# Optimization experiments

Hardware: AMD Instinct MI355X
Metric: run time of the kernel (lower is better)

## Reference

```python
import jax, jax.numpy as jnp
import numpy as np

D, H, NL, DFF, VS, VT = 512, 8, 6, 2048, 32000, 32000
B, SS, ST = 4, 512, 512
PAD = 1
EPS = 1e-5


def _pos_encoding(S, d):
    pos = jnp.arange(S, dtype=jnp.float32)[:, None]
    div = jnp.exp(jnp.arange(0, d, 2, dtype=jnp.float32) * (-jnp.log(jnp.float32(10000.0)) / d))
    pe = jnp.zeros((S, d), dtype=jnp.float32)
    pe = pe.at[:, 0::2].set(jnp.sin(pos * div))
    pe = pe.at[:, 1::2].set(jnp.cos(pos * div))
    return pe


def _ln(x, g, b):
    m = jnp.mean(x, axis=-1, keepdims=True)
    v = jnp.mean(jnp.square(x - m), axis=-1, keepdims=True)
    return (x - m) * jax.lax.rsqrt(v + EPS) * g + b


def _mha(q, k, v, Wq, Wk, Wv, Wo, mask):
    # q,k,v: [B,S,D]; W*: [D,D] (torch Linear: y = x @ W.T); mask True -> masked
    Bq, Sq, _ = q.shape
    Sk = k.shape[1]
    dk = D // H
    Q = (q @ Wq.T).reshape(Bq, Sq, H, dk).transpose(0, 2, 1, 3)
    K = (k @ Wk.T).reshape(Bq, Sk, H, dk).transpose(0, 2, 1, 3)
    V = (v @ Wv.T).reshape(Bq, Sk, H, dk).transpose(0, 2, 1, 3)
    scores = jnp.einsum('bhqd,bhkd->bhqk', Q, K) / jnp.sqrt(jnp.float32(dk))
    scores = jnp.where(mask, -jnp.inf, scores)
    w = jax.nn.softmax(scores, axis=-1)
    w = jnp.nan_to_num(w)  # matches torch.nan_to_num after softmax of all -inf rows
    out = jnp.einsum('bhqk,bhkd->bhqd', w, V)
    out = out.transpose(0, 2, 1, 3).reshape(Bq, Sq, D)
    return out @ Wo.T


def _ffn(x, w1, b1, w2, b2):
    return jax.nn.relu(x @ w1.T + b1) @ w2.T + b2


def setup_inputs() -> dict:
    key = jax.random.key(0)
    ks = jax.random.split(key, 48)
    i = iter(range(48))
    n = lambda shape, s=0.02: jax.random.normal(ks[next(i)], shape, dtype=jnp.float32) * s
    inp = {
        'src': jax.random.randint(ks[next(i)], (B, SS), 0, VS),
        'tgt': jax.random.randint(ks[next(i)], (B, ST), 0, VT),
        'src_embed': n((VS, D)),
        'tgt_embed': n((VT, D)),
        'enc_Wq': n((NL, D, D)), 'enc_Wk': n((NL, D, D)), 'enc_Wv': n((NL, D, D)), 'enc_Wo': n((NL, D, D)),
        'enc_w1': n((NL, DFF, D)), 'enc_b1': jnp.zeros((NL, DFF)),
        'enc_w2': n((NL, D, DFF)), 'enc_b2': jnp.zeros((NL, D)),
        'enc_ln1g': jnp.ones((NL, D)), 'enc_ln1b': jnp.zeros((NL, D)),
        'enc_ln2g': jnp.ones((NL, D)), 'enc_ln2b': jnp.zeros((NL, D)),
        'enc_lnfg': jnp.ones((D,)), 'enc_lnfb': jnp.zeros((D,)),
        'dec_sWq': n((NL, D, D)), 'dec_sWk': n((NL, D, D)), 'dec_sWv': n((NL, D, D)), 'dec_sWo': n((NL, D, D)),
        'dec_cWq': n((NL, D, D)), 'dec_cWk': n((NL, D, D)), 'dec_cWv': n((NL, D, D)), 'dec_cWo': n((NL, D, D)),
        'dec_w1': n((NL, DFF, D)), 'dec_b1': jnp.zeros((NL, DFF)),
        'dec_w2': n((NL, D, DFF)), 'dec_b2': jnp.zeros((NL, D)),
        'dec_ln1g': jnp.ones((NL, D)), 'dec_ln1b': jnp.zeros((NL, D)),
        'dec_ln2g': jnp.ones((NL, D)), 'dec_ln2b': jnp.zeros((NL, D)),
        'dec_ln3g': jnp.ones((NL, D)), 'dec_ln3b': jnp.zeros((NL, D)),
        'dec_lnfg': jnp.ones((D,)), 'dec_lnfb': jnp.zeros((D,)),
        'out_W': n((VT, D)), 'out_b': jnp.zeros((VT,)),
    }
    return inp


def reference(src, tgt, src_embed, tgt_embed,
              enc_Wq, enc_Wk, enc_Wv, enc_Wo, enc_w1, enc_b1, enc_w2, enc_b2,
              enc_ln1g, enc_ln1b, enc_ln2g, enc_ln2b, enc_lnfg, enc_lnfb,
              dec_sWq, dec_sWk, dec_sWv, dec_sWo, dec_cWq, dec_cWk, dec_cWv, dec_cWo,
              dec_w1, dec_b1, dec_w2, dec_b2,
              dec_ln1g, dec_ln1b, dec_ln2g, dec_ln2b, dec_ln3g, dec_ln3b,
              dec_lnfg, dec_lnfb, out_W, out_b):
    scale = jnp.sqrt(jnp.float32(D))
    src_mask = (src == PAD)[:, None, None, :]                      # [B,1,1,SS]
    causal = jnp.triu(jnp.ones((ST, ST), dtype=bool), k=1)[None, None]
    tgt_mask = (tgt == PAD)[:, None, None, :] | causal             # [B,1,ST,ST]

    # Encoder
    x = src_embed[src] * scale + _pos_encoding(SS, D)[None]
    for l in range(NL):
        nrm = _ln(x, enc_ln1g[l], enc_ln1b[l])
        x = x + _mha(nrm, nrm, nrm, enc_Wq[l], enc_Wk[l], enc_Wv[l], enc_Wo[l], src_mask)
        x = x + _ffn(_ln(x, enc_ln2g[l], enc_ln2b[l]), enc_w1[l], enc_b1[l], enc_w2[l], enc_b2[l])
    memory = _ln(x, enc_lnfg, enc_lnfb)

    # Decoder
    y = tgt_embed[tgt] * scale + _pos_encoding(ST, D)[None]
    for l in range(NL):
        nrm = _ln(y, dec_ln1g[l], dec_ln1b[l])
        y = y + _mha(nrm, nrm, nrm, dec_sWq[l], dec_sWk[l], dec_sWv[l], dec_sWo[l], tgt_mask)
        nrm = _ln(y, dec_ln2g[l], dec_ln2b[l])
        y = y + _mha(nrm, memory, memory, dec_cWq[l], dec_cWk[l], dec_cWv[l], dec_cWo[l], src_mask)
        y = y + _ffn(_ln(y, dec_ln3g[l], dec_ln3b[l]), dec_w1[l], dec_b1[l], dec_w2[l], dec_b2[l])
    y = _ln(y, dec_lnfg, dec_lnfb)

    logits = y @ out_W.T + out_b                                   # [B,ST,VT]
    return logits
```

## Files before the change

### kernel.cpp

```cpp
#include <hip/hip_runtime.h>
#include <hip/hip_bf16.h>
#include <math.h>

#define Dm    512
#define Hh    8
#define NLay  6
#define DFFm  2048
#define Bb    4
#define NTOK  2048
#define PADID 1
#define LNEPS 1e-5f
#define S2W   262144

typedef __attribute__((ext_vector_type(8))) short short8;
typedef __attribute__((ext_vector_type(4))) float f32x4;
typedef unsigned short u16;

__device__ __forceinline__ u16 f2bf(float f) {
    union { float f; unsigned int i; } x; x.f = f;
    unsigned int r = x.i + 0x7fffu + ((x.i >> 16) & 1u);
    return (u16)(r >> 16);
}

typedef const __attribute__((address_space(1))) void* as1cv;
typedef __attribute__((address_space(3))) void* as3v;
__device__ __forceinline__ void gl_lds16(const u16* g, u16* l) {
    __builtin_amdgcn_global_load_lds((as1cv)g, (as3v)l, 16, 0, 0);
}

__device__ __forceinline__ void swz_tile(int& mt, int& nt) {
    const int nwg  = gridDim.x * gridDim.y;
    const int orig = blockIdx.y * gridDim.x + blockIdx.x;
    const int q8 = nwg >> 3, r8 = nwg & 7;
    const int xcd = orig & 7, idx = orig >> 3;
    const int wgid = (xcd < r8 ? xcd * (q8 + 1) : r8 * (q8 + 1) + (xcd - r8) * q8) + idx;
    const int MT = gridDim.y;
    mt = wgid % MT;
    nt = wgid / MT;
}

struct CvtJobs {
    const float* s[17];
    u16*         d[17];
    long         n4[17];
};
__global__ __launch_bounds__(256) void cvt_many(CvtJobs j) {
    const int job = blockIdx.y;
    const long n4 = j.n4[job];
    const float* in = j.s[job];
    u16* out = j.d[job];
    long i = (long)blockIdx.x * 256 + threadIdx.x;
    const long stride = (long)gridDim.x * 256;
    for (; i < n4; i += stride) {
        float4 v = ((const float4*)in)[i];
        ushort4 o;
        o.x = f2bf(v.x); o.y = f2bf(v.y); o.z = f2bf(v.z); o.w = f2bf(v.w);
        ((ushort4*)out)[i] = o;
    }
}

__global__ __launch_bounds__(256) void gemm_bt(
    const u16* __restrict__ A, int lda,
    const u16* __restrict__ B0, const u16* __restrict__ B1,
    const u16* __restrict__ B2, int ldb,
    float* Cf, u16* Cb, int csm,
    const float* __restrict__ bias,
    const float* res, int ldres,
    int K, int vth, int koff, u16* vtp)
{
    __shared__ u16 As[2][2048];
    __shared__ u16 Bs[2][2048];
    int mt, nt; swz_tile(mt, nt);
    const int m0 = mt << 6, n0 = nt << 6;
    const int t = threadIdx.x, lane = t & 63, wave = t >> 6;
    const int wr = (wave >> 1) << 5, wc = (wave & 1) << 5;
    const int fr = lane & 15, fq = lane >> 4;
    const int srow = t >> 2;
    const int sch  = (t & 3) ^ (srow & 3);
    const u16* Bsel = (n0 < 512) ? B0 : (n0 < 1024 ? B1 : B2);
    const u16* Ag = A + (long)(m0 + srow) * lda + (sch << 3);
    const u16* Bg = Bsel + (long)((n0 & 511) + srow) * ldb + (sch << 3);

    f32x4 acc[2][2];
    #pragma unroll
    for (int i = 0; i < 2; i++)
        #pragma unroll
        for (int j = 0; j < 2; j++) acc[i][j] = (f32x4){0.f, 0.f, 0.f, 0.f};

    const int nk = K >> 5;
    gl_lds16(Ag, &As[0][t << 3]);
    gl_lds16(Bg, &Bs[0][t << 3]);
    for (int ki = 0; ki < nk; ki++) {
        const int cur = ki & 1;
        __syncthreads();
        if (ki + 1 < nk) {
            gl_lds16(Ag + ((ki + 1) << 5), &As[cur ^ 1][t << 3]);
            gl_lds16(Bg + ((ki + 1) << 5), &Bs[cur ^ 1][t << 3]);
        }
        const int r0 = wr + fr, r1 = wr + 16 + fr;
        const int c0 = wc + fr, c1 = wc + 16 + fr;
        short8 af0 = *(const short8*)&As[cur][(r0 << 5) + ((fq ^ (r0 & 3)) << 3)];
        short8 af1 = *(const short8*)&As[cur][(r1 << 5) + ((fq ^ (r1 & 3)) << 3)];
        short8 bf0 = *(const short8*)&Bs[cur][(c0 << 5) + ((fq ^ (c0 & 3)) << 3)];
        short8 bf1 = *(const short8*)&Bs[cur][(c1 << 5) + ((fq ^ (c1 & 3)) << 3)];
        acc[0][0] = __builtin_amdgcn_mfma_f32_16x16x32_bf16(af0, bf0, acc[0][0], 0, 0, 0);
        acc[0][1] = __builtin_amdgcn_mfma_f32_16x16x32_bf16(af0, bf1, acc[0][1], 0, 0, 0);
        acc[1][0] = __builtin_amdgcn_mfma_f32_16x16x32_bf16(af1, bf0, acc[1][0], 0, 0, 0);
        acc[1][1] = __builtin_amdgcn_mfma_f32_16x16x32_bf16(af1, bf1, acc[1][1], 0, 0, 0);
        __syncthreads();
    }

    #pragma unroll
    for (int i = 0; i < 2; i++) {
        #pragma unroll
        for (int j = 0; j < 2; j++) {
            const int nl  = n0 + wc + (j << 4) + fr;
            const int mlb = m0 + wr + (i << 4) + (fq << 2);
            const float bsv = bias ? bias[nl] : 0.f;
            #pragma unroll
            for (int r = 0; r < 4; r++) {
                const int ml = mlb + r;
                float v = acc[i][j][r] + bsv;
                if (nl >= vth) {
                    vtp[(long)(ml >> 9) * S2W + (long)(nl - vth) * 512 + (ml & 511)] = f2bf(v);
                } else {
                    long ci = (long)ml * csm + nl + koff;
                    if (res) v += res[(long)ml * ldres + nl];
                    if (Cf) Cf[ci] = v;
                    if (Cb) Cb[ci] = f2bf(v);
                }
            }
        }
    }
}

__global__ __launch_bounds__(256) void gemm_big(
    const u16* __restrict__ A, int lda,
    const u16* __restrict__ B, int ldb,
    float* Cf, u16* Cb, int ldc,
    const float* __restrict__ bias, int relu, int K)
{
    __shared__ u16 As[2][4096];
    __shared__ u16 Bs[2][4096];
    int mt, nt; swz_tile(mt, nt);
    const int m0 = mt << 7, n0 = nt << 7;
    const int t = threadIdx.x, lane = t & 63, wave = t >> 6;
    const int wr = (wave >> 1) << 6, wc = (wave & 1) << 6;
    const int fr = lane & 15, fq = lane >> 4;
    const int srow = t >> 2;
    const int sch  = (t & 3) ^ (srow & 3);
    const u16* Ag0 = A + (long)(m0 + srow) * lda + (sch << 3);
    const u16* Ag1 = A + (long)(m0 + 64 + srow) * lda + (sch << 3);
    const u16* Bg0 = B + (long)(n0 + srow) * ldb + (sch << 3);
    const u16* Bg1 = B + (long)(n0 + 64 + srow) * ldb + (sch << 3);

    f32x4 acc[4][4];
    #pragma unroll
    for (int i = 0; i < 4; i++)
        #pragma unroll
        for (int j = 0; j < 4; j++) acc[i][j] = (f32x4){0.f, 0.f, 0.f, 0.f};

    const int nk = K >> 5;
    gl_lds16(Ag0, &As[0][t << 3]);
    gl_lds16(Ag1, &As[0][2048 + (t << 3)]);
    gl_lds16(Bg0, &Bs[0][t << 3]);
    gl_lds16(Bg1, &Bs[0][2048 + (t << 3)]);
    for (int ki = 0; ki < nk; ki++) {
        const int cur = ki & 1;
        __syncthreads();
        if (ki + 1 < nk) {
            const int ko = (ki + 1) << 5;
            gl_lds16(Ag0 + ko, &As[cur ^ 1][t << 3]);
            gl_lds16(Ag1 + ko, &As[cur ^ 1][2048 + (t << 3)]);
            gl_lds16(Bg0 + ko, &Bs[cur ^ 1][t << 3]);
            gl_lds16(Bg1 + ko, &Bs[cur ^ 1][2048 + (t << 3)]);
        }
        short8 af[4], bf[4];
        #pragma unroll
        for (int i = 0; i < 4; i++) {
            const int r = wr + (i << 4) + fr;
            af[i] = *(const short8*)&As[cur][(r << 5) + ((fq ^ (r & 3)) << 3)];
        }
        #pragma unroll
        for (int j = 0; j < 4; j++) {
            const int c = wc + (j << 4) + fr;
            bf[j] = *(const short8*)&Bs[cur][(c << 5) + ((fq ^ (c & 3)) << 3)];
        }
        #pragma unroll
        for (int i = 0; i < 4; i++)
            #pragma unroll
            for (int j = 0; j < 4; j++)
                acc[i][j] = __builtin_amdgcn_mfma_f32_16x16x32_bf16(af[i], bf[j], acc[i][j], 0, 0, 0);
        __syncthreads();
    }

    #pragma unroll
    for (int i = 0; i < 4; i++) {
        #pragma unroll
        for (int j = 0; j < 4; j++) {
            const int nl  = n0 + wc + (j << 4) + fr;
            const int mlb = m0 + wr + (i << 4) + (fq << 2);
            const float bsv = bias ? bias[nl] : 0.f;
            #pragma unroll
            for (int r = 0; r < 4; r++) {
                float v = acc[i][j][r] + bsv;
                if (relu) v = fmaxf(v, 0.f);
                long ci = (long)(mlb + r) * ldc + nl;
                if (Cf) Cf[ci] = v;
                if (Cb) Cb[ci] = f2bf(v);
            }
        }
    }
}

__global__ __launch_bounds__(256) void attn_fused(
    const u16* __restrict__ qkb, const u16* __restrict__ vt,
    const int* __restrict__ ids, u16* __restrict__ attc, int causal)
{
    __shared__ u16 Ks[2][4096];
    __shared__ u16 Vs[2][4096];
    __shared__ short Ps[4][16][72];
    const int t = threadIdx.x, lane = t & 63, w = t >> 6;
    const int fr = lane & 15, fq = lane >> 4;
    const int q0 = blockIdx.x << 6, h = blockIdx.y, b = blockIdx.z;

    const u16* qp = qkb + (long)(b * 512 + q0 + (w << 4) + fr) * 1024 + h * 64 + (fq << 3);
    short8 aq0 = *(const short8*)qp;
    short8 aq1 = *(const short8*)(qp + 32);

    const int sr0 = t >> 3,        sc0 = (t & 7) ^ (sr0 & 7);
    const int sr1 = (t + 256) >> 3, sc1 = ((t + 256) & 7) ^ (sr1 & 7);
    const u16* kg0 = qkb + (long)(b * 512 + sr0) * 1024 + 512 + h * 64 + (sc0 << 3);
    const u16* kg1 = qkb + (long)(b * 512 + sr1) * 1024 + 512 + h * 64 + (sc1 << 3);
    const u16* vg0 = vt + (long)b * S2W + (long)(h * 64 + sr0) * 512 + (sc0 << 3);
    const u16* vg1 = vt + (long)b * S2W + (long)(h * 64 + sr1) * 512 + (sc1 << 3);

    unsigned pmask = 0;
    #pragma unroll
    for (int kt = 0; kt < 8; kt++)
        #pragma unroll
        for (int j = 0; j < 4; j++)
            if (ids[b * 512 + (kt << 6) + (j << 4) + fr] == PADID)
                pmask |= 1u << ((kt << 2) + j);

    float m[4], l[4]; f32x4 oc[4];
    #pragma unroll
    for (int r = 0; r < 4; r++) { m[r] = -INFINITY; l[r] = 0.f; oc[r] = (f32x4){0.f,0.f,0.f,0.f}; }

    const int lastkt = causal ? (q0 >> 6) : 7;
    auto stage = [&](int kt, int buf) {
        const long so = (long)(kt << 6);
        gl_lds16(kg0 + so * 1024, &Ks[buf][t << 3]);
        gl_lds16(kg1 + so * 1024, &Ks[buf][(t + 256) << 3]);
        gl_lds16(vg0 + so, &Vs[buf][t << 3]);
        gl_lds16(vg1 + so, &Vs[buf][(t + 256) << 3]);
    };
    stage(0, 0);

    for (int kt = 0; kt <= lastkt; kt++) {
        const int cur = kt & 1;
        __syncthreads();
        if (kt < lastkt) stage(kt + 1, cur ^ 1);

        f32x4 sc[4];
        #pragma unroll
        for (int j = 0; j < 4; j++) sc[j] = (f32x4){0.f,0.f,0.f,0.f};
        #pragma unroll
        for (int j = 0; j < 4; j++) {
            const int rr = (j << 4) + fr;
            short8 bk0 = *(const short8*)&Ks[cur][rr * 64 + ((fq ^ (rr & 7)) << 3)];
            short8 bk1 = *(const short8*)&Ks[cur][rr * 64 + (((fq | 4) ^ (rr & 7)) << 3)];
            sc[j] = __builtin_amdgcn_mfma_f32_16x16x32_bf16(aq0, bk0, sc[j], 0, 0, 0);
            sc[j] = __builtin_amdgcn_mfma_f32_16x16x32_bf16(aq1, bk1, sc[j], 0, 0, 0);
        }
        const int s0 = kt << 6;
        #pragma unroll
        for (int r = 0; r < 4; r++) {
            const int qa = q0 + (w << 4) + (fq << 2) + r;
            float mx = -INFINITY;
            #pragma unroll
            for (int j = 0; j < 4; j++) {
                bool msk = ((pmask >> ((kt << 2) + j)) & 1) ||
                           (causal && (s0 + (j << 4) + fr) > qa);
                float sv = msk ? -INFINITY : sc[j][r] * 0.125f;
                sc[j][r] = sv;
                mx = fmaxf(mx, sv);
            }
            mx = fmaxf(mx, __shfl_xor(mx, 1)); mx = fmaxf(mx, __shfl_xor(mx, 2));
            mx = fmaxf(mx, __shfl_xor(mx, 4)); mx = fmaxf(mx, __shfl_xor(mx, 8));
            float mnew  = fmaxf(m[r], mx);
            float scale = (mnew == -INFINITY) ? 1.f : __expf(m[r] - mnew);
            float ps = 0.f;
            #pragma unroll
            for (int j = 0; j < 4; j++) {
                float p = (sc[j][r] == -INFINITY) ? 0.f : __expf(sc[j][r] - mnew);
                sc[j][r] = p; ps += p;
            }
            ps += __shfl_xor(ps, 1); ps += __shfl_xor(ps, 2);
            ps += __shfl_xor(ps, 4); ps += __shfl_xor(ps, 8);
            l[r] = l[r] * scale + ps;
            m[r] = mnew;
            #pragma unroll
            for (int j2 = 0; j2 < 4; j2++) oc[j2][r] *= scale;
        }
        #pragma unroll
        for (int r = 0; r < 4; r++)
            #pragma unroll
            for (int j = 0; j < 4; j++)
                Ps[w][(fq << 2) + r][(j << 4) + fr] = (short)f2bf(sc[j][r]);
        #pragma unroll
        for (int kc = 0; kc < 2; kc++) {
            short8 pa = *(const short8*)&Ps[w][fr][(kc << 5) + (fq << 3)];
            #pragma unroll
            for (int j2 = 0; j2 < 4; j2++) {
                const int rd = (j2 << 4) + fr;
                const int cch = (((kc << 2) | fq) ^ (rd & 7));
                short8 bv = *(const short8*)&Vs[cur][rd * 64 + (cch << 3)];
                oc[j2] = __builtin_amdgcn_mfma_f32_16x16x32_bf16(pa, bv, oc[j2], 0, 0, 0);
            }
        }
        __syncthreads();
    }

    float inv[4];
    #pragma unroll
    for (int r = 0; r < 4; r++) inv[r] = (l[r] > 0.f) ? 1.f / l[r] : 0.f;
    #pragma unroll
    for (int j2 = 0; j2 < 4; j2++)
        #pragma unroll
        for (int r = 0; r < 4; r++)
            attc[(long)(b * 512 + q0 + (w << 4) + (fq << 2) + r) * 512 + h * 64 + (j2 << 4) + fr]
                = f2bf(oc[j2][r] * inv[r]);
}

__global__ __launch_bounds__(256) void ln_rows(
    const float* __restrict__ x, const float* __restrict__ g,
    const float* __restrict__ b, u16* __restrict__ out)
{
    int row  = blockIdx.x * 4 + (threadIdx.x >> 6);
    int lane = threadIdx.x & 63;
    const float* xr = x + (long)row * Dm;
    float v[8]; float s = 0.f;
    #pragma unroll
    for (int i = 0; i < 8; i++) { v[i] = xr[lane + (i << 6)]; s += v[i]; }
    #pragma unroll
    for (int o = 32; o > 0; o >>= 1) s += __shfl_xor(s, o);
    float mean = s * (1.f / 512.f);
    float q = 0.f;
    #pragma unroll
    for (int i = 0; i < 8; i++) { float d = v[i] - mean; q += d * d; }
    #pragma unroll
    for (int o = 32; o > 0; o >>= 1) q += __shfl_xor(q, o);
    float rinv = rsqrtf(q * (1.f / 512.f) + LNEPS);
    u16* orow = out + (long)row * Dm;
    #pragma unroll
    for (int i = 0; i < 8; i++) {
        int c = lane + (i << 6);
        orow[c] = f2bf((v[i] - mean) * rinv * g[c] + b[c]);
    }
}

__global__ __launch_bounds__(256) void embed_pe(
    const int* __restrict__ ids, const float* __restrict__ emb,
    float* __restrict__ out)
{
    int idx = blockIdx.x * 256 + threadIdx.x;
    int d   = idx & 511;
    int tok = idx >> 9;
    int s   = tok & 511;
    int id  = ids[tok];
    float val = emb[(long)id * Dm + d] * 22.62741699796952f;
    int i2 = d >> 1;
    float dv  = expf((float)(i2 << 1) * (-9.210340371976184f / 512.f));
    float ang = (float)s * dv;
    val += (d & 1) ? cosf(ang) : sinf(ang);
    out[idx] = val;
}

extern "C" void kernel_launch(void* const* d_in, const int* in_sizes, int n_in,
                              void* d_out, int out_size, void* d_ws, size_t ws_size,
                              hipStream_t stream)
{
    (void)in_sizes; (void)n_in; (void)out_size; (void)ws_size;
    const int*   src       = (const int*)d_in[0];
    const int*   tgt       = (const int*)d_in[1];
    const float* src_embed = (const float*)d_in[2];
    const float* tgt_embed = (const float*)d_in[3];
    const float* enc_b1  = (const float*)d_in[9];
    const float* enc_b2  = (const float*)d_in[11];
    const float* enc_ln1g = (const float*)d_in[12];
    const float* enc_ln1b = (const float*)d_in[13];
    const float* enc_ln2g = (const float*)d_in[14];
    const float* enc_ln2b = (const float*)d_in[15];
    const float* enc_lnfg = (const float*)d_in[16];
    const float* enc_lnfb = (const float*)d_in[17];
    const float* dec_b1  = (const float*)d_in[27];
    const float* dec_b2  = (const float*)d_in[29];
    const float* dec_ln1g = (const float*)d_in[30];
    const float* dec_ln1b = (const float*)d_in[31];
    const float* dec_ln2g = (const float*)d_in[32];
    const float* dec_ln2b = (const float*)d_in[33];
    const float* dec_ln3g = (const float*)d_in[34];
    const float* dec_ln3b = (const float*)d_in[35];
    const float* dec_lnfg = (const float*)d_in[36];
    const float* dec_lnfb = (const float*)d_in[37];
    const float* out_b  = (const float*)d_in[39];

    char* wp = (char*)d_ws;
    auto carve = [&](size_t nbytes) {
        void* p = (void*)wp; wp += (nbytes + 255) & ~(size_t)255; return p;
    };

    const long nW = (long)NLay * S2W;
    const long nF = (long)NLay * DFFm * Dm;
    const long nO = 32000L * Dm;

    u16* Wb[12];
    for (int i = 0; i < 12; i++) Wb[i] = (u16*)carve((size_t)nW * 2);
    u16* w1E  = (u16*)carve((size_t)nF * 2);
    u16* w2E  = (u16*)carve((size_t)nF * 2);
    u16* w1D  = (u16*)carve((size_t)nF * 2);
    u16* w2D  = (u16*)carve((size_t)nF * 2);
    u16* outW = (u16*)carve((size_t)nO * 2);

    float* x  = (float*)carve((size_t)NTOK * Dm * 4);
    float* y  = (float*)carve((size_t)NTOK * Dm * 4);
    u16* nrm  = (u16*)carve((size_t)NTOK * Dm * 2);
    u16* qkb  = (u16*)carve((size_t)NTOK * 1024 * 2);
    u16* vt   = (u16*)carve((size_t)Bb * Dm * 512 * 2);
    u16* attc = (u16*)carve((size_t)NTOK * Dm * 2);
    u16* h1   = (u16*)carve((size_t)NTOK * DFFm * 2);
    u16* memn = (u16*)carve((size_t)NTOK * Dm * 2);

    const int wi[12] = {4, 5, 6, 7, 18, 19, 20, 21, 22, 23, 24, 25};
    CvtJobs jobs;
    for (int i = 0; i < 12; i++) {
        jobs.s[i] = (const float*)d_in[wi[i]]; jobs.d[i] = Wb[i]; jobs.n4[i] = nW >> 2;
    }
    jobs.s[12] = (const float*)d_in[8];  jobs.d[12] = w1E;  jobs.n4[12] = nF >> 2;
    jobs.s[13] = (const float*)d_in[10]; jobs.d[13] = w2E;  jobs.n4[13] = nF >> 2;
    jobs.s[14] = (const float*)d_in[26]; jobs.d[14] = w1D;  jobs.n4[14] = nF >> 2;
    jobs.s[15] = (const float*)d_in[28]; jobs.d[15] = w2D;  jobs.n4[15] = nF >> 2;
    jobs.s[16] = (const float*)d_in[38]; jobs.d[16] = outW; jobs.n4[16] = nO >> 2;
    cvt_many<<<dim3(512, 17), 256, 0, stream>>>(jobs);

    const int BIG = 1 << 28;
    u16 *eWq = Wb[0], *eWk = Wb[1], *eWv = Wb[2], *eWo = Wb[3];
    u16 *sWq = Wb[4], *sWk = Wb[5], *sWv = Wb[6], *sWo = Wb[7];
    u16 *cWq = Wb[8], *cWk = Wb[9], *cWv = Wb[10], *cWo = Wb[11];

    embed_pe<<<4096, 256, 0, stream>>>(src, src_embed, x);
    for (int l = 0; l < NLay; l++) {
        const size_t wo = (size_t)l * S2W;
        ln_rows<<<512, 256, 0, stream>>>(x, enc_ln1g + l * Dm, enc_ln1b + l * Dm, nrm);
        gemm_bt<<<dim3(24, 32), 256, 0, stream>>>(nrm, 512, eWq + wo, eWk + wo, eWv + wo, 512,
            nullptr, qkb, 1024, nullptr, nullptr, 0, 512, 1024, 0, vt);
        attn_fused<<<dim3(8, Hh, Bb), 256, 0, stream>>>(qkb, vt, src, attc, 0);
        gemm_bt<<<dim3(8, 32), 256, 0, stream>>>(attc, 512, eWo + wo, nullptr, nullptr, 512,
            x, nullptr, 512, nullptr, x, 512, 512, BIG, 0, nullptr);
        ln_rows<<<512, 256, 0, stream>>>(x, enc_ln2g + l * Dm, enc_ln2b + l * Dm, nrm);
        gemm_big<<<dim3(16, 16), 256, 0, stream>>>(nrm, 512, w1E + (size_t)l * DFFm * Dm, 512,
            nullptr, h1, DFFm, enc_b1 + l * DFFm, 1, 512);
        gemm_bt<<<dim3(8, 32), 256, 0, stream>>>(h1, DFFm, w2E + (size_t)l * Dm * DFFm,
            nullptr, nullptr, DFFm, x, nullptr, 512, enc_b2 + l * Dm, x, 512, 2048, BIG, 0, nullptr);
    }
    ln_rows<<<512, 256, 0, stream>>>(x, enc_lnfg, enc_lnfb, memn);

    embed_pe<<<4096, 256, 0, stream>>>(tgt, tgt_embed, y);
    for (int l = 0; l < NLay; l++) {
        const size_t wo = (size_t)l * S2W;
        ln_rows<<<512, 256, 0, stream>>>(y, dec_ln1g + l * Dm, dec_ln1b + l * Dm, nrm);
        gemm_bt<<<dim3(24, 32), 256, 0, stream>>>(nrm, 512, sWq + wo, sWk + wo, sWv + wo, 512,
            nullptr, qkb, 1024, nullptr, nullptr, 0, 512, 1024, 0, vt);
        attn_fused<<<dim3(8, Hh, Bb), 256, 0, stream>>>(qkb, vt, tgt, attc, 1);
        gemm_bt<<<dim3(8, 32), 256, 0, stream>>>(attc, 512, sWo + wo, nullptr, nullptr, 512,
            y, nullptr, 512, nullptr, y, 512, 512, BIG, 0, nullptr);
        ln_rows<<<512, 256, 0, stream>>>(y, dec_ln2g + l * Dm, dec_ln2b + l * Dm, nrm);
        gemm_bt<<<dim3(8, 32), 256, 0, stream>>>(nrm, 512, cWq + wo, nullptr, nullptr, 512,
            nullptr, qkb, 1024, nullptr, nullptr, 0, 512, BIG, 0, nullptr);
        gemm_bt<<<dim3(16, 32), 256, 0, stream>>>(memn, 512, cWk + wo, cWv + wo, nullptr, 512,
            nullptr, qkb, 1024, nullptr, nullptr, 0, 512, 512, 512, vt);
        attn_fused<<<dim3(8, Hh, Bb), 256, 0, stream>>>(qkb, vt, src, attc, 0);
        gemm_bt<<<dim3(8, 32), 256, 0, stream>>>(attc, 512, cWo + wo, nullptr, nullptr, 512,
            y, nullptr, 512, nullptr, y, 512, 512, BIG, 0, nullptr);
        ln_rows<<<512, 256, 0, stream>>>(y, dec_ln3g + l * Dm, dec_ln3b + l * Dm, nrm);
        gemm_big<<<dim3(16, 16), 256, 0, stream>>>(nrm, 512, w1D + (size_t)l * DFFm * Dm, 512,
            nullptr, h1, DFFm, dec_b1 + l * DFFm, 1, 512);
        gemm_bt<<<dim3(8, 32), 256, 0, stream>>>(h1, DFFm, w2D + (size_t)l * Dm * DFFm,
            nullptr, nullptr, DFFm, y, nullptr, 512, dec_b2 + l * Dm, y, 512, 2048, BIG, 0, nullptr);
    }
    ln_rows<<<512, 256, 0, stream>>>(y, dec_lnfg, dec_lnfb, nrm);

    gemm_big<<<dim3(250, 16), 256, 0, stream>>>(nrm, 512, outW, 512,
        (float*)d_out, nullptr, 32000, out_b, 0, 512);
}
```

Measured before the change: 1.919 ms.

## Deepen gemm_bt K-tile to 64, fix LDS swizzle, drop redundant loop syncs

gemm_bt now stages a 64-wide K slice per iteration, using an 8-chunk XOR swizzle, which halves the number of loop iterations and barriers. gemm_big's swizzle now keys on row>>1 to avoid LDS bank conflicts for its 32-wide rows. In gemm_bt, gemm_big and attention, the barrier at the top of the loop is replaced by a single barrier after the prologue, so each iteration keeps only its trailing sync. LDS use in gemm_bt doubles, which may reduce occupancy.

```diff
diff --git a/kernel.cpp b/kernel.cpp
--- a/kernel.cpp
+++ b/kernel.cpp
@@ -68,18 +68,20 @@
     const float* res, int ldres,
     int K, int vth, int koff, u16* vtp)
 {
-    __shared__ u16 As[2][2048];
-    __shared__ u16 Bs[2][2048];
+    __shared__ u16 As[2][4096];
+    __shared__ u16 Bs[2][4096];
     int mt, nt; swz_tile(mt, nt);
     const int m0 = mt << 6, n0 = nt << 6;
     const int t = threadIdx.x, lane = t & 63, wave = t >> 6;
     const int wr = (wave >> 1) << 5, wc = (wave & 1) << 5;
     const int fr = lane & 15, fq = lane >> 4;
-    const int srow = t >> 2;
-    const int sch  = (t & 3) ^ (srow & 3);
+    const int srow = t >> 3;
+    const int sch  = (t & 7) ^ (srow & 7);
     const u16* Bsel = (n0 < 512) ? B0 : (n0 < 1024 ? B1 : B2);
-    const u16* Ag = A + (long)(m0 + srow) * lda + (sch << 3);
-    const u16* Bg = Bsel + (long)((n0 & 511) + srow) * ldb + (sch << 3);
+    const u16* Ag0 = A + (long)(m0 + srow) * lda + (sch << 3);
+    const u16* Ag1 = A + (long)(m0 + 32 + srow) * lda + (sch << 3);
+    const u16* Bg0 = Bsel + (long)((n0 & 511) + srow) * ldb + (sch << 3);
+    const u16* Bg1 = Bsel + (long)((n0 & 511) + 32 + srow) * ldb + (sch << 3);
 
     f32x4 acc[2][2];
     #pragma unroll
@@ -87,26 +89,35 @@
         #pragma unroll
         for (int j = 0; j < 2; j++) acc[i][j] = (f32x4){0.f, 0.f, 0.f, 0.f};
 
-    const int nk = K >> 5;
-    gl_lds16(Ag, &As[0][t << 3]);
-    gl_lds16(Bg, &Bs[0][t << 3]);
+    const int nk = K >> 6;
+    gl_lds16(Ag0, &As[0][t << 3]);
+    gl_lds16(Ag1, &As[0][(t + 256) << 3]);
+    gl_lds16(Bg0, &Bs[0][t << 3]);
+    gl_lds16(Bg1, &Bs[0][(t + 256) << 3]);
+    __syncthreads();
     for (int ki = 0; ki < nk; ki++) {
         const int cur = ki & 1;
-        __syncthreads();
         if (ki + 1 < nk) {
-            gl_lds16(Ag + ((ki + 1) << 5), &As[cur ^ 1][t << 3]);
-            gl_lds16(Bg + ((ki + 1) << 5), &Bs[cur ^ 1][t << 3]);
+            const int ko = (ki + 1) << 6;
+            gl_lds16(Ag0 + ko, &As[cur ^ 1][t << 3]);
+            gl_lds16(Ag1 + ko, &As[cur ^ 1][(t + 256) << 3]);
+            gl_lds16(Bg0 + ko, &Bs[cur ^ 1][t << 3]);
+            gl_lds16(Bg1 + ko, &Bs[cur ^ 1][(t + 256) << 3]);
         }
         const int r0 = wr + fr, r1 = wr + 16 + fr;
         const int c0 = wc + fr, c1 = wc + 16 + fr;
-        short8 af0 = *(const short8*)&As[cur][(r0 << 5) + ((fq ^ (r0 & 3)) << 3)];
-        short8 af1 = *(const short8*)&As[cur][(r1 << 5) + ((fq ^ (r1 & 3)) << 3)];
-        short8 bf0 = *(const short8*)&Bs[cur][(c0 << 5) + ((fq ^ (c0 & 3)) << 3)];
-        short8 bf1 = *(const short8*)&Bs[cur][(c1 << 5) + ((fq ^ (c1 & 3)) << 3)];
-        acc[0][0] = __builtin_amdgcn_mfma_f32_16x16x32_bf16(af0, bf0, acc[0][0], 0, 0, 0);
-        acc[0][1] = __builtin_amdgcn_mfma_f32_16x16x32_bf16(af0, bf1, acc[0][1], 0, 0, 0);
-        acc[1][0] = __builtin_amdgcn_mfma_f32_16x16x32_bf16(af1, bf0, acc[1][0], 0, 0, 0);
-        acc[1][1] = __builtin_amdgcn_mfma_f32_16x16x32_bf16(af1, bf1, acc[1][1], 0, 0, 0);
+        #pragma unroll
+        for (int h = 0; h < 2; h++) {
+            const int lc = fq | (h << 2);
+            short8 af0 = *(const short8*)&As[cur][(r0 << 6) + ((lc ^ (r0 & 7)) << 3)];
+            short8 af1 = *(const short8*)&As[cur][(r1 << 6) + ((lc ^ (r1 & 7)) << 3)];
+            short8 bf0 = *(const short8*)&Bs[cur][(c0 << 6) + ((lc ^ (c0 & 7)) << 3)];
+            short8 bf1 = *(const short8*)&Bs[cur][(c1 << 6) + ((lc ^ (c1 & 7)) << 3)];
+            acc[0][0] = __builtin_amdgcn_mfma_f32_16x16x32_bf16(af0, bf0, acc[0][0], 0, 0, 0);
+            acc[0][1] = __builtin_amdgcn_mfma_f32_16x16x32_bf16(af0, bf1, acc[0][1], 0, 0, 0);
+            acc[1][0] = __builtin_amdgcn_mfma_f32_16x16x32_bf16(af1, bf0, acc[1][0], 0, 0, 0);
+            acc[1][1] = __builtin_amdgcn_mfma_f32_16x16x32_bf16(af1, bf1, acc[1][1], 0, 0, 0);
+        }
         __syncthreads();
     }
 
@@ -148,7 +159,7 @@
     const int wr = (wave >> 1) << 6, wc = (wave & 1) << 6;
     const int fr = lane & 15, fq = lane >> 4;
     const int srow = t >> 2;
-    const int sch  = (t & 3) ^ (srow & 3);
+    const int sch  = (t & 3) ^ ((srow >> 1) & 3);
     const u16* Ag0 = A + (long)(m0 + srow) * lda + (sch << 3);
     const u16* Ag1 = A + (long)(m0 + 64 + srow) * lda + (sch << 3);
     const u16* Bg0 = B + (long)(n0 + srow) * ldb + (sch << 3);
@@ -162,29 +173,29 @@
 
     const int nk = K >> 5;
     gl_lds16(Ag0, &As[0][t << 3]);
-    gl_lds16(Ag1, &As[0][2048 + (t << 3)]);
+    gl_lds16(Ag1, &As[0][(t + 256) << 3]);
     gl_lds16(Bg0, &Bs[0][t << 3]);
-    gl_lds16(Bg1, &Bs[0][2048 + (t << 3)]);
+    gl_lds16(Bg1, &Bs[0][(t + 256) << 3]);
+    __syncthreads();
     for (int ki = 0; ki < nk; ki++) {
         const int cur = ki & 1;
-        __syncthreads();
         if (ki + 1 < nk) {
             const int ko = (ki + 1) << 5;
             gl_lds16(Ag0 + ko, &As[cur ^ 1][t << 3]);
-            gl_lds16(Ag1 + ko, &As[cur ^ 1][2048 + (t << 3)]);
+            gl_lds16(Ag1 + ko, &As[cur ^ 1][(t + 256) << 3]);
             gl_lds16(Bg0 + ko, &Bs[cur ^ 1][t << 3]);
-            gl_lds16(Bg1 + ko, &Bs[cur ^ 1][2048 + (t << 3)]);
+            gl_lds16(Bg1 + ko, &Bs[cur ^ 1][(t + 256) << 3]);
         }
         short8 af[4], bf[4];
         #pragma unroll
         for (int i = 0; i < 4; i++) {
             const int r = wr + (i << 4) + fr;
-            af[i] = *(const short8*)&As[cur][(r << 5) + ((fq ^ (r & 3)) << 3)];
+            af[i] = *(const short8*)&As[cur][(r << 5) + ((fq ^ ((r >> 1) & 3)) << 3)];
         }
         #pragma unroll
         for (int j = 0; j < 4; j++) {
             const int c = wc + (j << 4) + fr;
-            bf[j] = *(const short8*)&Bs[cur][(c << 5) + ((fq ^ (c & 3)) << 3)];
+            bf[j] = *(const short8*)&Bs[cur][(c << 5) + ((fq ^ ((c >> 1) & 3)) << 3)];
         }
         #pragma unroll
         for (int i = 0; i < 4; i++)
@@ -228,12 +239,11 @@
     short8 aq0 = *(const short8*)qp;
     short8 aq1 = *(const short8*)(qp + 32);
 
-    const int sr0 = t >> 3,        sc0 = (t & 7) ^ (sr0 & 7);
-    const int sr1 = (t + 256) >> 3, sc1 = ((t + 256) & 7) ^ (sr1 & 7);
-    const u16* kg0 = qkb + (long)(b * 512 + sr0) * 1024 + 512 + h * 64 + (sc0 << 3);
-    const u16* kg1 = qkb + (long)(b * 512 + sr1) * 1024 + 512 + h * 64 + (sc1 << 3);
-    const u16* vg0 = vt + (long)b * S2W + (long)(h * 64 + sr0) * 512 + (sc0 << 3);
-    const u16* vg1 = vt + (long)b * S2W + (long)(h * 64 + sr1) * 512 + (sc1 << 3);
+    const int sr = t >> 3, sc = (t & 7) ^ (sr & 7);
+    const u16* kg0 = qkb + (long)(b * 512 + sr) * 1024 + 512 + h * 64 + (sc << 3);
+    const u16* kg1 = kg0 + 32L * 1024;
+    const u16* vg0 = vt + (long)b * S2W + (long)(h * 64 + sr) * 512 + (sc << 3);
+    const u16* vg1 = vg0 + 32L * 512;
 
     unsigned pmask = 0;
     #pragma unroll
@@ -256,22 +266,22 @@
         gl_lds16(vg1 + so, &Vs[buf][(t + 256) << 3]);
     };
     stage(0, 0);
+    __syncthreads();
 
     for (int kt = 0; kt <= lastkt; kt++) {
         const int cur = kt & 1;
-        __syncthreads();
         if (kt < lastkt) stage(kt + 1, cur ^ 1);
 
-        f32x4 sc[4];
-        #pragma unroll
-        for (int j = 0; j < 4; j++) sc[j] = (f32x4){0.f,0.f,0.f,0.f};
+        f32x4 sc4[4];
+        #pragma unroll
+        for (int j = 0; j < 4; j++) sc4[j] = (f32x4){0.f,0.f,0.f,0.f};
         #pragma unroll
         for (int j = 0; j < 4; j++) {
             const int rr = (j << 4) + fr;
             short8 bk0 = *(const short8*)&Ks[cur][rr * 64 + ((fq ^ (rr & 7)) << 3)];
             short8 bk1 = *(const short8*)&Ks[cur][rr * 64 + (((fq | 4) ^ (rr & 7)) << 3)];
-            sc[j] = __builtin_amdgcn_mfma_f32_16x16x32_bf16(aq0, bk0, sc[j], 0, 0, 0);
-            sc[j] = __builtin_amdgcn_mfma_f32_16x16x32_bf16(aq1, bk1, sc[j], 0, 0, 0);
+            sc4[j] = __builtin_amdgcn_mfma_f32_16x16x32_bf16(aq0, bk0, sc4[j], 0, 0, 0);
+            sc4[j] = __builtin_amdgcn_mfma_f32_16x16x32_bf16(aq1, bk1, sc4[j], 0, 0, 0);
         }
         const int s0 = kt << 6;
         #pragma unroll
@@ -282,8 +292,8 @@
             for (int j = 0; j < 4; j++) {
                 bool msk = ((pmask >> ((kt << 2) + j)) & 1) ||
                            (causal && (s0 + (j << 4) + fr) > qa);
-                float sv = msk ? -INFINITY : sc[j][r] * 0.125f;
-                sc[j][r] = sv;
+                float sv = msk ? -INFINITY : sc4[j][r] * 0.125f;
+                sc4[j][r] = sv;
                 mx = fmaxf(mx, sv);
             }
             mx = fmaxf(mx, __shfl_xor(mx, 1)); mx = fmaxf(mx, __shfl_xor(mx, 2));
@@ -293,8 +303,8 @@
             float ps = 0.f;
             #pragma unroll
             for (int j = 0; j < 4; j++) {
-                float p = (sc[j][r] == -INFINITY) ? 0.f : __expf(sc[j][r] - mnew);
-                sc[j][r] = p; ps += p;
+                float p = (sc4[j][r] == -INFINITY) ? 0.f : __expf(sc4[j][r] - mnew);
+                sc4[j][r] = p; ps += p;
             }
             ps += __shfl_xor(ps, 1); ps += __shfl_xor(ps, 2);
             ps += __shfl_xor(ps, 4); ps += __shfl_xor(ps, 8);
@@ -307,7 +317,7 @@
         for (int r = 0; r < 4; r++)
             #pragma unroll
             for (int j = 0; j < 4; j++)
-                Ps[w][(fq << 2) + r][(j << 4) + fr] = (short)f2bf(sc[j][r]);
+                Ps[w][(fq << 2) + r][(j << 4) + fr] = (short)f2bf(sc4[j][r]);
         #pragma unroll
         for (int kc = 0; kc < 2; kc++) {
             short8 pa = *(const short8*)&Ps[w][fr][(kc << 5) + (fq << 3)];
```

Measured after the change: 1.857 ms. 3.2% less time.
